# Kernel tuning notes

Hardware: AMD Instinct MI355X
Metric: run time of the kernel (lower is better)

## Reference

```python
import jax, jax.numpy as jnp
import numpy as np

EPS = 1e-5

def _ln(x, g, b):
    m = x.mean(-1, keepdims=True)
    v = jnp.var(x, axis=-1, keepdims=True)
    return (x - m) * jax.lax.rsqrt(v + EPS) * g + b

def _conv(x, w, b, stride=1, pad=1):
    y = jax.lax.conv_general_dilated(x, w, (stride, stride), [(pad, pad), (pad, pad)],
                                     dimension_numbers=('NCHW', 'OIHW', 'NCHW'))
    return y + b[None, :, None, None]

def _bn(x, g, b, m, v):
    # inference-mode BatchNorm2d
    inv = jax.lax.rsqrt(v + EPS)
    return (x - m[None, :, None, None]) * (g * inv)[None, :, None, None] + b[None, :, None, None]

def _sru_dir(u0, u1, u2, res, vf, vr, bf, br, reverse):
    # elementwise gated recurrence (SRU v2, identity activation, no dropout)
    def step(c, inp):
        a0, a1, a2, rx = inp
        f = jax.nn.sigmoid(a1 + vf * c + bf)
        c2 = f * c + (1.0 - f) * a0
        r = jax.nn.sigmoid(a2 + vr * c2 + br)
        return c2, r * c2 + (1.0 - r) * rx
    c0 = jnp.zeros_like(u0[0])
    _, hs = jax.lax.scan(step, c0, (u0, u1, u2, res), reverse=reverse)
    return hs

def _sru_layer(x, g, b, wp, w, vc, bias, k, h):
    # x: [L,B,n_in]; layer_norm on input, factored weight (projection), bidirectional
    xn = _ln(x, g, b)
    L, B, _ = xn.shape
    U = (xn @ wp) @ w                      # [L,B,2*k*h]
    U = U.reshape(L, B, 2, k, h)
    outs = []
    for d, rev in ((0, False), (1, True)):
        u = U[:, :, d]
        res = u[..., 3, :] if k == 4 else xn[..., d * h:(d + 1) * h]
        outs.append(_sru_dir(u[..., 0, :], u[..., 1, :], u[..., 2, :], res,
                             vc[d, 0], vc[d, 1], bias[d, 0], bias[d, 1], rev))
    return jnp.concatenate(outs, axis=-1)

def _forward(x, conv0_w, conv0_b, rconv1_w, rconv1_b, rbn1_g, rbn1_b, rbn1_m, rbn1_v,
             rconv2_w, rconv2_b, rbn2_g, rbn2_b, rbn2_m, rbn2_v,
             ln0_g, ln0_b, wproj0, w0, vc0, bias0, ln_g, ln_b, wproj, w, vc, bias,
             cln_g, cln_b, cls_w):
    H = 512
    h = _conv(x, conv0_w, conv0_b, stride=2)           # [B,32,F/2,T/2]
    for i in range(3):                                  # 3 residual blocks
        r = h
        h1 = jax.nn.relu(_bn(_conv(h, rconv1_w[i], rconv1_b[i]), rbn1_g[i], rbn1_b[i], rbn1_m[i], rbn1_v[i]))
        h2 = _bn(_conv(h1, rconv2_w[i], rconv2_b[i]), rbn2_g[i], rbn2_b[i], rbn2_m[i], rbn2_v[i])
        h = jax.nn.relu(h2 + r)
    Bb, C, Fr, Tt = h.shape
    s = h.reshape(Bb, C * Fr, Tt).transpose(2, 0, 1)   # [T,B,2048]
    s = _sru_layer(s, ln0_g, ln0_b, wproj0, w0, vc0, bias0, 4, H)  # layer 0: n_in != n_out -> k=4
    for i in range(3):                                  # layers 1..3: n_in == n_out -> k=3
        s = _sru_layer(s, ln_g[i], ln_b[i], wproj[i], w[i], vc[i], bias[i], 3, H)
    s = s.transpose(1, 0, 2)                            # [B,T,1024]
    s = _ln(s, cln_g, cln_b)
    return s @ cls_w                                    # [B,T,30]

def setup_inputs():
    key = jax.random.key(0)
    ks = iter(jax.random.split(key, 32))
    def nrm(shape, scale=1.0):
        return jax.random.normal(next(ks), shape, jnp.float32) * scale
    H, P, F2, D, hb = 512, 256, 2048, 1024, -2.0
    d = {}
    d['x'] = nrm((16, 1, 128, 2048))
    d['conv0_w'] = nrm((32, 1, 3, 3), (2.0 / 9) ** 0.5)
    d['conv0_b'] = jnp.zeros((32,))
    d['rconv1_w'] = nrm((3, 32, 32, 3, 3), (2.0 / (32 * 9)) ** 0.5)
    d['rconv1_b'] = jnp.zeros((3, 32))
    d['rbn1_g'] = jnp.ones((3, 32)); d['rbn1_b'] = jnp.zeros((3, 32))
    d['rbn1_m'] = nrm((3, 32), 0.1); d['rbn1_v'] = jnp.ones((3, 32))
    d['rconv2_w'] = nrm((3, 32, 32, 3, 3), (2.0 / (32 * 9)) ** 0.5)
    d['rconv2_b'] = jnp.zeros((3, 32))
    d['rbn2_g'] = 0.1 * jnp.ones((3, 32)); d['rbn2_b'] = jnp.zeros((3, 32))
    d['rbn2_m'] = nrm((3, 32), 0.1); d['rbn2_v'] = jnp.ones((3, 32))
    d['ln0_g'] = jnp.ones((F2,)); d['ln0_b'] = jnp.zeros((F2,))
    d['wproj0'] = nrm((F2, P), F2 ** -0.5)
    d['w0'] = nrm((P, 2 * 4 * H), P ** -0.5)
    d['vc0'] = nrm((2, 2, H), 0.1)
    d['bias0'] = jnp.zeros((2, 2, H)).at[:, 0].set(hb)
    d['ln_g'] = jnp.ones((3, D)); d['ln_b'] = jnp.zeros((3, D))
    d['wproj'] = nrm((3, D, P), D ** -0.5)
    d['w'] = nrm((3, P, 2 * 3 * H), P ** -0.5)
    d['vc'] = nrm((3, 2, 2, H), 0.1)
    d['bias'] = jnp.zeros((3, 2, 2, H)).at[:, :, 0].set(hb)
    d['cln_g'] = jnp.ones((D,)); d['cln_b'] = jnp.zeros((D,))
    d['cls_w'] = nrm((D, 30), D ** -0.5)
    return d

def reference(x, conv0_w, conv0_b, rconv1_w, rconv1_b, rbn1_g, rbn1_b, rbn1_m, rbn1_v,
              rconv2_w, rconv2_b, rbn2_g, rbn2_b, rbn2_m, rbn2_v,
              ln0_g, ln0_b, wproj0, w0, vc0, bias0, ln_g, ln_b, wproj, w, vc, bias,
              cln_g, cln_b, cls_w):
    return _forward(x, conv0_w, conv0_b, rconv1_w, rconv1_b, rbn1_g, rbn1_b, rbn1_m, rbn1_v,
                    rconv2_w, rconv2_b, rbn2_g, rbn2_b, rbn2_m, rbn2_v,
                    ln0_g, ln0_b, wproj0, w0, vc0, bias0, ln_g, ln_b, wproj, w, vc, bias,
                    cln_g, cln_b, cls_w)
```

## Files before the change

kernel.cpp:

```cpp
#include <hip/hip_runtime.h>
#include <hip/hip_bf16.h>
#include <math.h>

#define DEV __device__ __forceinline__

typedef __attribute__((ext_vector_type(8))) short short8;
typedef __attribute__((ext_vector_type(4))) float floatx4;

DEV float b2f_lo(unsigned u) { return __uint_as_float(u << 16); }
DEV float b2f_hi(unsigned u) { return __uint_as_float(u & 0xffff0000u); }

#if __has_builtin(__builtin_amdgcn_exp2f)
DEV float fexp2_(float x) { return __builtin_amdgcn_exp2f(x); }
#else
DEV float fexp2_(float x) { return exp2f(x); }
#endif
#if __has_builtin(__builtin_amdgcn_rcpf)
DEV float frcp_(float x) { return __builtin_amdgcn_rcpf(x); }
#else
DEV float frcp_(float x) { return 1.f / x; }
#endif

DEV void gl2lds16(const void* g, void* l) {
  __builtin_amdgcn_global_load_lds(
      (const __attribute__((address_space(1))) unsigned int*)g,
      (__attribute__((address_space(3))) unsigned int*)l, 16, 0, 0);
}

union U8 { uint4 u; __hip_bfloat16 h[8]; };

__global__ __launch_bounds__(256) void conv_stem_nhwc(const float* __restrict__ x,
    const float* __restrict__ w, const float* __restrict__ bias,
    __hip_bfloat16* __restrict__ out) {
  __shared__ float sX[3][2052];
  __shared__ float sW[288];
  __shared__ float sB[32];
  const int tid = threadIdx.x;
  const int f = blockIdx.x, n = blockIdx.y;
  const float* xb = x + (size_t)n * 262144;

  for (int i = tid; i < 1536; i += 256) {
    int r = i >> 9, c4 = i & 511;
    int fi = 2 * f - 1 + r;
    float4 v = {0.f, 0.f, 0.f, 0.f};
    if (fi >= 0 && fi < 128) v = *(const float4*)&xb[fi * 2048 + c4 * 4];
    sX[r][1 + c4 * 4 + 0] = v.x;
    sX[r][1 + c4 * 4 + 1] = v.y;
    sX[r][1 + c4 * 4 + 2] = v.z;
    sX[r][1 + c4 * 4 + 3] = v.w;
  }
  if (tid < 3) { sX[tid][0] = 0.f; sX[tid][2049] = 0.f; }
  for (int i = tid; i < 288; i += 256) sW[i] = w[i];
  if (tid < 32) sB[tid] = bias[tid];
  __syncthreads();

  float xv[4][9];
#pragma unroll
  for (int q = 0; q < 4; ++q) {
    int t = tid + q * 256;
#pragma unroll
    for (int r = 0; r < 3; ++r)
#pragma unroll
      for (int dc = 0; dc < 3; ++dc)
        xv[q][r * 3 + dc] = sX[r][2 * t + dc];
  }
#pragma unroll
  for (int ocq = 0; ocq < 4; ++ocq) {
    float wr[8][9];
#pragma unroll
    for (int oo = 0; oo < 8; ++oo)
#pragma unroll
      for (int qq = 0; qq < 9; ++qq)
        wr[oo][qq] = sW[(ocq * 8 + oo) * 9 + qq];
#pragma unroll
    for (int q = 0; q < 4; ++q) {
      U8 o;
#pragma unroll
      for (int oo = 0; oo < 8; ++oo) {
        float acc = sB[ocq * 8 + oo];
#pragma unroll
        for (int qq = 0; qq < 9; ++qq) acc = fmaf(wr[oo][qq], xv[q][qq], acc);
        o.h[oo] = __float2bfloat16(acc);
      }
      int t = tid + q * 256;
      *(uint4*)&out[(((size_t)n * 64 + f) * 1024 + t) * 32 + ocq * 8] = o.u;
    }
  }
}

__global__ __launch_bounds__(256) void wtap_conv6(const float* __restrict__ w1,
    const float* __restrict__ w2, __hip_bfloat16* __restrict__ out) {
  int i = blockIdx.x * 256 + threadIdx.x;
  if (i < 55296) {
    int b = i / 9216, r = i - b * 9216;
    int layer = b >> 1, which = b & 1;
    const float* src = (which ? w2 : w1) + layer * 9216;
    int tap = r >> 10, oc = (r >> 5) & 31, ic = r & 31;
    out[b * 9216 + r] = __float2bfloat16(src[(oc * 32 + ic) * 9 + tap]);
  }
}

template <int ADD>
__global__ __launch_bounds__(256) void conv_mfma(const __hip_bfloat16* __restrict__ Hin,
    const __hip_bfloat16* __restrict__ wt,
    const float* __restrict__ cb, const float* __restrict__ bg,
    const float* __restrict__ bb, const float* __restrict__ bm,
    const float* __restrict__ bv, __hip_bfloat16* Hres) {
  __shared__ __hip_bfloat16 sIn[6 * 66 * 40];
  __hip_bfloat16* sOut = sIn;
  const int tid = threadIdx.x;
  const int tb = blockIdx.x, fb = blockIdx.y, n = blockIdx.z;
  const int t0 = tb * 64, f0 = fb * 4;
  const __hip_bfloat16* Hb = Hin + (size_t)n * 2097152;

  for (int c = tid; c < 1584; c += 256) {
    int rr = c / 264;
    int r2 = c - rr * 264;
    int p = r2 >> 2, icq = r2 & 3;
    int fi = f0 - 1 + rr;
    int tg = t0 + p - 1;
    uint4 v = {0, 0, 0, 0};
    if (fi >= 0 && fi < 64 && tg >= 0 && tg < 1024)
      v = *(const uint4*)&Hb[((size_t)fi * 1024 + tg) * 32 + icq * 8];
    *(uint4*)&sIn[(rr * 66 + p) * 40 + icq * 8] = v;
  }

  const int lane = tid & 63, wave = tid >> 6;
  const int fr = lane & 15, fq = lane >> 4;
  short8 bfrag[9][2];
#pragma unroll
  for (int tap = 0; tap < 9; ++tap)
#pragma unroll
    for (int j = 0; j < 2; ++j)
      bfrag[tap][j] = *(const short8*)&wt[(tap * 32 + j * 16 + fr) * 32 + fq * 8];

  __syncthreads();

  const int tw = wave * 16;
  floatx4 acc[4][2];
#pragma unroll
  for (int fp = 0; fp < 4; ++fp)
#pragma unroll
    for (int j = 0; j < 2; ++j) acc[fp][j] = (floatx4){0.f, 0.f, 0.f, 0.f};

#pragma unroll
  for (int fp = 0; fp < 4; ++fp) {
    int pbase = tw + fr;
#pragma unroll
    for (int df = 0; df < 3; ++df)
#pragma unroll
      for (int dc = 0; dc < 3; ++dc) {
        short8 af =
            *(const short8*)&sIn[((fp + df) * 66 + pbase + dc) * 40 + fq * 8];
        acc[fp][0] = __builtin_amdgcn_mfma_f32_16x16x32_bf16(
            af, bfrag[df * 3 + dc][0], acc[fp][0], 0, 0, 0);
        acc[fp][1] = __builtin_amdgcn_mfma_f32_16x16x32_bf16(
            af, bfrag[df * 3 + dc][1], acc[fp][1], 0, 0, 0);
      }
  }

  float sc0 = bg[fr] * rsqrtf(bv[fr] + 1e-5f);
  float sh0 = (cb[fr] - bm[fr]) * sc0 + bb[fr];
  float sc1 = bg[fr + 16] * rsqrtf(bv[fr + 16] + 1e-5f);
  float sh1 = (cb[fr + 16] - bm[fr + 16]) * sc1 + bb[fr + 16];

  __syncthreads();
#pragma unroll
  for (int fp = 0; fp < 4; ++fp)
#pragma unroll
    for (int j = 0; j < 2; ++j) {
      float sc = j ? sc1 : sc0, sh = j ? sh1 : sh0;
#pragma unroll
      for (int reg = 0; reg < 4; ++reg) {
        int t_l = tw + fq * 4 + reg;
        sOut[(fp * 64 + t_l) * 40 + j * 16 + fr] =
            __float2bfloat16(acc[fp][j][reg] * sc + sh);
      }
    }
  __syncthreads();

  for (int c = tid; c < 1024; c += 256) {
    int fp = c >> 8, rem = c & 255;
    int t_l = rem >> 2, icq = rem & 3;
    U8 y;
    y.u = *(uint4*)&sOut[(fp * 64 + t_l) * 40 + icq * 8];
    size_t addr = (((size_t)n * 64 + f0 + fp) * 1024 + t0 + t_l) * 32 + icq * 8;
    U8 o;
    if (ADD) {
      U8 r;
      r.u = *(const uint4*)&Hres[addr];
#pragma unroll
      for (int i = 0; i < 8; ++i)
        o.h[i] = __float2bfloat16(
            fmaxf(__bfloat162float(y.h[i]) + __bfloat162float(r.h[i]), 0.f));
    } else {
#pragma unroll
      for (int i = 0; i < 8; ++i)
        o.h[i] = __float2bfloat16(fmaxf(__bfloat162float(y.h[i]), 0.f));
    }
    *(uint4*)&Hres[addr] = o.u;
  }
}

__global__ __launch_bounds__(256) void ln_nhwc(const __hip_bfloat16* __restrict__ H,
    const float* __restrict__ g, const float* __restrict__ b,
    __hip_bfloat16* __restrict__ xn) {
  int r = blockIdx.x;
  int t = r >> 4, n = r & 15;
  int tid = threadIdx.x;
  int f = tid >> 2, icq = tid & 3;
  U8 v;
  v.u = *(const uint4*)&H[(((size_t)n * 64 + f) * 1024 + t) * 32 + icq * 8];
  float xv[8];
  float sum = 0.f, ss = 0.f;
#pragma unroll
  for (int i = 0; i < 8; ++i) {
    xv[i] = __bfloat162float(v.h[i]);
    sum += xv[i];
    ss += xv[i] * xv[i];
  }
#pragma unroll
  for (int off = 32; off > 0; off >>= 1) {
    sum += __shfl_down(sum, off);
    ss  += __shfl_down(ss, off);
  }
  __shared__ float red[8];
  int lane = tid & 63, wave = tid >> 6;
  if (lane == 0) { red[wave] = sum; red[4 + wave] = ss; }
  __syncthreads();
  sum = red[0] + red[1] + red[2] + red[3];
  ss  = red[4] + red[5] + red[6] + red[7];
  float mean = sum * (1.f / 2048.f);
  float var = ss * (1.f / 2048.f) - mean * mean;
  float inv = rsqrtf(var + 1e-5f);
  U8 o;
#pragma unroll
  for (int i = 0; i < 8; ++i) {
    int cf = (icq * 8 + i) * 64 + f;
    o.h[i] = __float2bfloat16((xv[i] - mean) * inv * g[cf] + b[cf]);
  }
  *(uint4*)&xn[(size_t)r * 2048 + tid * 8] = o.u;
}

__global__ __launch_bounds__(256) void wt_perm0(const float* __restrict__ in,
    __hip_bfloat16* __restrict__ out) {
  int i = blockIdx.x * 256 + threadIdx.x;
  int p = i >> 11, kp = i & 2047;
  int ic = kp & 31, f = kp >> 5;
  out[i] = __float2bfloat16(in[(ic * 64 + f) * 256 + p]);
}

__global__ __launch_bounds__(256) void ln_rows_h(const __hip_bfloat16* __restrict__ in,
    const float* __restrict__ g, const float* __restrict__ b,
    __hip_bfloat16* __restrict__ out) {
  int r = blockIdx.x;
  int tid = threadIdx.x;
  union { ushort4 u; __hip_bfloat16 h[4]; } iv;
  iv.u = *(const ushort4*)&in[(size_t)r * 1024 + tid * 4];
  float x0 = __bfloat162float(iv.h[0]);
  float x1 = __bfloat162float(iv.h[1]);
  float x2 = __bfloat162float(iv.h[2]);
  float x3 = __bfloat162float(iv.h[3]);
  float sum = x0 + x1 + x2 + x3;
  float ss = x0 * x0 + x1 * x1 + x2 * x2 + x3 * x3;
#pragma unroll
  for (int off = 32; off > 0; off >>= 1) {
    sum += __shfl_down(sum, off);
    ss  += __shfl_down(ss, off);
  }
  __shared__ float red[8];
  int lane = tid & 63, wave = tid >> 6;
  if (lane == 0) { red[wave] = sum; red[4 + wave] = ss; }
  __syncthreads();
  sum = red[0] + red[1] + red[2] + red[3];
  ss  = red[4] + red[5] + red[6] + red[7];
  float mean = sum * (1.f / 1024.f);
  float var = ss * (1.f / 1024.f) - mean * mean;
  float inv = rsqrtf(var + 1e-5f);
  float4 gv = *(const float4*)&g[tid * 4];
  float4 bv = *(const float4*)&b[tid * 4];
  union { ushort4 u; __hip_bfloat16 h[4]; } o;
  o.h[0] = __float2bfloat16((x0 - mean) * inv * gv.x + bv.x);
  o.h[1] = __float2bfloat16((x1 - mean) * inv * gv.y + bv.y);
  o.h[2] = __float2bfloat16((x2 - mean) * inv * gv.z + bv.z);
  o.h[3] = __float2bfloat16((x3 - mean) * inv * gv.w + bv.w);
  *(ushort4*)&out[(size_t)r * 1024 + tid * 4] = o.u;
}

__global__ __launch_bounds__(256) void wt_bf16(const float* __restrict__ in,
    __hip_bfloat16* __restrict__ out, int K, int N, int inStride, int outStride) {
  __shared__ float tile[32][33];
  int x = threadIdx.x, y0 = threadIdx.y;
  int bn = blockIdx.x * 32;
  int bk = blockIdx.y * 32;
  const float* src = in + (size_t)blockIdx.z * inStride;
  __hip_bfloat16* dst = out + (size_t)blockIdx.z * outStride;
#pragma unroll
  for (int i = 0; i < 4; ++i) {
    int yy = y0 + i * 8;
    tile[yy][x] = src[(size_t)(bk + yy) * N + bn + x];
  }
  __syncthreads();
#pragma unroll
  for (int i = 0; i < 4; ++i) {
    int yy = y0 + i * 8;
    dst[(size_t)(bn + yy) * K + bk + x] = __float2bfloat16(tile[x][yy]);
  }
}

__global__ void wexp_prep(const float* __restrict__ in,
    __hip_bfloat16* __restrict__ out, int korig, int inStride, int outStride) {
  __shared__ float tile[32][33];
  int jt = blockIdx.x;
  int ckt = blockIdx.y;
  int z = blockIdx.z;
  int layer = z >> 3, dk = z & 7;
  int d = dk >> 2, k = dk & 3;
  if (k >= korig) return;
  const float* src = in + (size_t)layer * inStride;
  __hip_bfloat16* dst = out + (size_t)layer * outStride;
  int x = threadIdx.x, y0 = threadIdx.y;
#pragma unroll
  for (int i = 0; i < 4; ++i) {
    int yy = y0 + i * 8;
    tile[yy][x] = src[(size_t)(ckt * 32 + yy) * (korig * 1024) +
                      (d * korig + k) * 512 + jt * 32 + x];
  }
  __syncthreads();
#pragma unroll
  for (int i = 0; i < 4; ++i) {
    int yy = y0 + i * 8;
    int j = jt * 32 + yy;
    int rIdx;
    if (korig == 4)
      rIdx = (d * 512 + j) * 4 + k;
    else
      rIdx = (k < 2) ? ((d * 512 + j) * 2 + k) : (2048 + d * 512 + j);
    dst[(size_t)rIdx * 256 + ckt * 32 + x] = __float2bfloat16(tile[x][yy]);
  }
}

__global__ __launch_bounds__(256) void wct_prep(const float* __restrict__ in,
    __hip_bfloat16* __restrict__ out) {
  int i = blockIdx.x * 256 + threadIdx.x;
  int nn = i >> 10, kk = i & 1023;
  out[i] = __float2bfloat16(nn < 30 ? in[kk * 30 + nn] : 0.f);
}

__global__ __launch_bounds__(256) void gemm_bf16(const __hip_bfloat16* __restrict__ A,
    const __hip_bfloat16* __restrict__ Bt, __hip_bfloat16* __restrict__ C,
    int M, int N, int K) {
  __shared__ __hip_bfloat16 As[128 * 32];
  __shared__ __hip_bfloat16 Bs[128 * 32];
  const int tid = threadIdx.x;
  const int m0 = blockIdx.y * 128, n0 = blockIdx.x * 128;
  const int lane = tid & 63, wave = tid >> 6;
  const int wm = wave & 1, wn = wave >> 1;
  const int fr = lane & 15, fq = lane >> 4;
  const int srow = lane >> 2, sch = lane & 3;

  const __hip_bfloat16* ga0 = &A[(size_t)(m0 + wave * 32 + srow) * K + sch * 8];
  const __hip_bfloat16* ga1 = ga0 + (size_t)16 * K;
  const __hip_bfloat16* gb0 = &Bt[(size_t)(n0 + wave * 32 + srow) * K + sch * 8];
  const __hip_bfloat16* gb1 = gb0 + (size_t)16 * K;
  __hip_bfloat16* la0 = &As[(wave * 32) * 32];
  __hip_bfloat16* la1 = &As[(wave * 32 + 16) * 32];
  __hip_bfloat16* lb0 = &Bs[(wave * 32) * 32];
  __hip_bfloat16* lb1 = &Bs[(wave * 32 + 16) * 32];

  floatx4 acc[4][4];
#pragma unroll
  for (int i = 0; i < 4; ++i)
#pragma unroll
    for (int j = 0; j < 4; ++j)
      acc[i][j] = (floatx4){0.f, 0.f, 0.f, 0.f};

  for (int k0 = 0; k0 < K; k0 += 32) {
    __syncthreads();
    gl2lds16(ga0 + k0, la0);
    gl2lds16(ga1 + k0, la1);
    gl2lds16(gb0 + k0, lb0);
    gl2lds16(gb1 + k0, lb1);
    __syncthreads();

    short8 af[4], bf_[4];
#pragma unroll
    for (int i = 0; i < 4; ++i) {
      af[i]  = *(const short8*)&As[(wm * 64 + i * 16 + fr) * 32 + fq * 8];
      bf_[i] = *(const short8*)&Bs[(wn * 64 + i * 16 + fr) * 32 + fq * 8];
    }
#pragma unroll
    for (int i = 0; i < 4; ++i)
#pragma unroll
      for (int j = 0; j < 4; ++j)
        acc[i][j] = __builtin_amdgcn_mfma_f32_16x16x32_bf16(af[i], bf_[j],
                                                            acc[i][j], 0, 0, 0);
  }

#pragma unroll
  for (int i = 0; i < 4; ++i)
#pragma unroll
    for (int j = 0; j < 4; ++j)
#pragma unroll
      for (int reg = 0; reg < 4; ++reg) {
        int row = m0 + wm * 64 + i * 16 + fq * 4 + reg;
        int col = n0 + wn * 64 + j * 16 + fr;
        C[(size_t)row * N + col] = __float2bfloat16(acc[i][j][reg]);
      }
}

__global__ __launch_bounds__(256) void cls_gemm(const __hip_bfloat16* __restrict__ A,
    const __hip_bfloat16* __restrict__ Wct, float* __restrict__ out) {
  const int tid = threadIdx.x;
  const int lane = tid & 63, wave = tid >> 6;
  const int fr = lane & 15, fq = lane >> 4;
  const int m0 = (blockIdx.x * 4 + wave) * 16;
  floatx4 acc[2];
  acc[0] = (floatx4){0.f, 0.f, 0.f, 0.f};
  acc[1] = (floatx4){0.f, 0.f, 0.f, 0.f};
#pragma unroll 4
  for (int k0 = 0; k0 < 1024; k0 += 32) {
    short8 af = *(const short8*)&A[(size_t)(m0 + fr) * 1024 + k0 + fq * 8];
    short8 b0 = *(const short8*)&Wct[(size_t)fr * 1024 + k0 + fq * 8];
    short8 b1 = *(const short8*)&Wct[(size_t)(16 + fr) * 1024 + k0 + fq * 8];
    acc[0] = __builtin_amdgcn_mfma_f32_16x16x32_bf16(af, b0, acc[0], 0, 0, 0);
    acc[1] = __builtin_amdgcn_mfma_f32_16x16x32_bf16(af, b1, acc[1], 0, 0, 0);
  }
#pragma unroll
  for (int j = 0; j < 2; ++j) {
    int col = j * 16 + fr;
    if (col < 30) {
#pragma unroll
      for (int reg = 0; reg < 4; ++reg) {
        int row = m0 + fq * 4 + reg;
        int t = row >> 4, n = row & 15;
        out[(size_t)n * 30720 + t * 30 + col] = acc[j][reg];
      }
    }
  }
}

__global__ __launch_bounds__(64) void sru_scan4(const __hip_bfloat16* __restrict__ U,
    const float* __restrict__ vc, const float* __restrict__ bias,
    __hip_bfloat16* __restrict__ out) {
  int gid = blockIdx.x * 64 + threadIdx.x;
  int j = gid & 511;
  int n = (gid >> 9) & 15;
  int d = gid >> 13;
  const float NL2E = -1.44269504f;
  float vf2 = NL2E * vc[(d * 2 + 0) * 512 + j];
  float vr2 = NL2E * vc[(d * 2 + 1) * 512 + j];
  float bf2 = NL2E * bias[(d * 2 + 0) * 512 + j];
  float br2 = NL2E * bias[(d * 2 + 1) * 512 + j];

  const char* Ub = (const char*)(U + (size_t)n * 4096 + d * 2048) + (size_t)j * 8;
  char* Ob = (char*)(out + (size_t)n * 1024 + d * 512) + (size_t)j * 2;
  const int US = d ? -131072 : 131072;
  const int OS = d ? -32768 : 32768;
  int uoff = d ? 1023 * 131072 : 0;
  int ooff = d ? 1023 * 32768 : 0;

  uint2 B0[16], B1[16], B2[16], B3[16];
  float c = 0.f;

#define LOADC(UB)                                                         \
  {                                                                       \
    _Pragma("unroll") for (int ss = 0; ss < 16; ++ss) {                   \
      UB[ss] = *(const uint2*)(Ub + uoff);                                \
      uoff += US;                                                         \
    }                                                                     \
  }

#define COMPC(UB)                                                         \
  {                                                                       \
    _Pragma("unroll") for (int ss = 0; ss < 16; ++ss) {                   \
      uint2 uv = UB[ss];                                                  \
      float a0 = b2f_lo(uv.x), a1 = b2f_hi(uv.x), a2 = b2f_lo(uv.y);      \
      float rx = b2f_hi(uv.y);                                            \
      float A1 = fmaf(a1, NL2E, bf2);                                     \
      float f = frcp_(1.f + fexp2_(fmaf(vf2, c, A1)));                    \
      float c2 = fmaf(f, c - a0, a0);                                     \
      float A2 = fmaf(a2, NL2E, br2);                                     \
      float r = frcp_(1.f + fexp2_(fmaf(vr2, c2, A2)));                   \
      float y = fmaf(r, c2 - rx, rx);                                     \
      *(__hip_bfloat16*)(Ob + ooff) = __float2bfloat16(y);                \
      ooff += OS;                                                         \
      c = c2;                                                             \
    }                                                                     \
  }

  LOADC(B0);
  LOADC(B1);
  LOADC(B2);
  for (int cb = 0; cb < 64; cb += 4) {
    LOADC(B3);
    COMPC(B0);
    if (cb + 4 < 64) LOADC(B0);
    COMPC(B1);
    if (cb + 5 < 64) LOADC(B1);
    COMPC(B2);
    if (cb + 6 < 64) LOADC(B2);
    COMPC(B3);
  }
#undef LOADC
#undef COMPC
}

__global__ __launch_bounds__(64) void sru_scan3(const __hip_bfloat16* __restrict__ U,
    const __hip_bfloat16* __restrict__ xn,
    const float* __restrict__ vc, const float* __restrict__ bias,
    __hip_bfloat16* __restrict__ out) {
  int gid = blockIdx.x * 64 + threadIdx.x;
  int j = gid & 511;
  int n = (gid >> 9) & 15;
  int d = gid >> 13;
  const float NL2E = -1.44269504f;
  float vf2 = NL2E * vc[(d * 2 + 0) * 512 + j];
  float vr2 = NL2E * vc[(d * 2 + 1) * 512 + j];
  float bf2 = NL2E * bias[(d * 2 + 0) * 512 + j];
  float br2 = NL2E * bias[(d * 2 + 1) * 512 + j];

  const char* Ub01 = (const char*)U + (size_t)n * 6144 + (size_t)(d * 512 + j) * 4;
  const char* Ub2  = (const char*)U + (size_t)n * 6144 +
                     (size_t)(2048 + d * 512 + j) * 2;
  const char* Xb = (const char*)xn + (size_t)n * 2048 + (size_t)(d * 512 + j) * 2;
  char* Ob = (char*)(out + (size_t)n * 1024 + d * 512) + (size_t)j * 2;
  const int US = d ? -98304 : 98304;
  const int XS = d ? -32768 : 32768;
  const int OS = d ? -32768 : 32768;
  int uoff = d ? 1023 * 98304 : 0;
  int u2off = uoff;
  int xoff = d ? 1023 * 32768 : 0;
  int ooff = xoff;

  uint B0u[16], B1u[16], B2u[16], B3u[16];
  ushort B0a[16], B1a[16], B2a[16], B3a[16];
  ushort B0x[16], B1x[16], B2x[16], B3x[16];
  float c = 0.f;

#define LOADC(Bu, Ba, Bx)                                                 \
  {                                                                       \
    _Pragma("unroll") for (int ss = 0; ss < 16; ++ss) {                   \
      Bu[ss] = *(const uint*)(Ub01 + uoff);                               \
      Ba[ss] = *(const ushort*)(Ub2 + u2off);                             \
      Bx[ss] = *(const ushort*)(Xb + xoff);                               \
      uoff += US;                                                         \
      u2off += US;                                                        \
      xoff += XS;                                                         \
    }                                                                     \
  }

#define COMPC(Bu, Ba, Bx)                                                 \
  {                                                                       \
    _Pragma("unroll") for (int ss = 0; ss < 16; ++ss) {                   \
      float a0 = b2f_lo(Bu[ss]), a1 = b2f_hi(Bu[ss]);                     \
      float a2 = __uint_as_float((uint)Ba[ss] << 16);                     \
      float rx = __uint_as_float((uint)Bx[ss] << 16);                     \
      float A1 = fmaf(a1, NL2E, bf2);                                     \
      float f = frcp_(1.f + fexp2_(fmaf(vf2, c, A1)));                    \
      float c2 = fmaf(f, c - a0, a0);                                     \
      float A2 = fmaf(a2, NL2E, br2);                                     \
      float r = frcp_(1.f + fexp2_(fmaf(vr2, c2, A2)));                   \
      float y = fmaf(r, c2 - rx, rx);                                     \
      *(__hip_bfloat16*)(Ob + ooff) = __float2bfloat16(y);                \
      ooff += OS;                                                         \
      c = c2;                                                             \
    }                                                                     \
  }

  LOADC(B0u, B0a, B0x);
  LOADC(B1u, B1a, B1x);
  LOADC(B2u, B2a, B2x);
  for (int cb = 0; cb < 64; cb += 4) {
    LOADC(B3u, B3a, B3x);
    COMPC(B0u, B0a, B0x);
    if (cb + 4 < 64) LOADC(B0u, B0a, B0x);
    COMPC(B1u, B1a, B1x);
    if (cb + 5 < 64) LOADC(B1u, B1a, B1x);
    COMPC(B2u, B2a, B2x);
    if (cb + 6 < 64) LOADC(B2u, B2a, B2x);
    COMPC(B3u, B3a, B3x);
  }
#undef LOADC
#undef COMPC
}

extern "C" void kernel_launch(void* const* d_in, const int* in_sizes, int n_in,
                              void* d_out, int out_size, void* d_ws, size_t ws_size,
                              hipStream_t stream) {
  const float* x        = (const float*)d_in[0];
  const float* conv0_w  = (const float*)d_in[1];
  const float* conv0_b  = (const float*)d_in[2];
  const float* rconv1_w = (const float*)d_in[3];
  const float* rconv1_b = (const float*)d_in[4];
  const float* rbn1_g   = (const float*)d_in[5];
  const float* rbn1_b   = (const float*)d_in[6];
  const float* rbn1_m   = (const float*)d_in[7];
  const float* rbn1_v   = (const float*)d_in[8];
  const float* rconv2_w = (const float*)d_in[9];
  const float* rconv2_b = (const float*)d_in[10];
  const float* rbn2_g   = (const float*)d_in[11];
  const float* rbn2_b   = (const float*)d_in[12];
  const float* rbn2_m   = (const float*)d_in[13];
  const float* rbn2_v   = (const float*)d_in[14];
  const float* ln0_g    = (const float*)d_in[15];
  const float* ln0_b    = (const float*)d_in[16];
  const float* wproj0   = (const float*)d_in[17];
  const float* w0       = (const float*)d_in[18];
  const float* vc0      = (const float*)d_in[19];
  const float* bias0    = (const float*)d_in[20];
  const float* ln_g     = (const float*)d_in[21];
  const float* ln_b     = (const float*)d_in[22];
  const float* wproj    = (const float*)d_in[23];
  const float* w        = (const float*)d_in[24];
  const float* vc       = (const float*)d_in[25];
  const float* bias     = (const float*)d_in[26];
  const float* cln_g    = (const float*)d_in[27];
  const float* cln_b    = (const float*)d_in[28];
  const float* cls_w    = (const float*)d_in[29];
  float* out = (float*)d_out;

  float* Af = (float*)d_ws;
  float* Bf = Af + 33554432;
  __hip_bfloat16* Ah = (__hip_bfloat16*)Af;
  __hip_bfloat16* Bh = (__hip_bfloat16*)Bf;

  __hip_bfloat16* hA     = Ah;
  __hip_bfloat16* hB     = Bh;
  __hip_bfloat16* wt_all = Ah + 62914560;
  __hip_bfloat16* Wp0t   = Ah + 52428800;

  __hip_bfloat16* s2h  = Bh;
  __hip_bfloat16* xnc  = Bh + 16777216;
  __hip_bfloat16* xn3  = Bh + 33554432;
  __hip_bfloat16* tmp  = Bh + 50331648;
  __hip_bfloat16* W3p  = Bh + 54525952;
  __hip_bfloat16* W0p  = Bh + 57671680;
  __hip_bfloat16* Wpt3 = Bh + 58720256;
  __hip_bfloat16* xn0  = Bh;
  __hip_bfloat16* U    = Ah;
  __hip_bfloat16* Wct  = Ah;

  wtap_conv6<<<216, 256, 0, stream>>>(rconv1_w, rconv2_w, wt_all);
  wt_perm0<<<2048, 256, 0, stream>>>(wproj0, Wp0t);
  wexp_prep<<<dim3(16, 8, 8), dim3(32, 8), 0, stream>>>(w0, W0p, 4, 0, 0);
  wexp_prep<<<dim3(16, 8, 24), dim3(32, 8), 0, stream>>>(w, W3p, 3,
                                                         786432, 786432);
  wt_bf16<<<dim3(8, 32, 3), dim3(32, 8), 0, stream>>>(wproj, Wpt3, 1024, 256,
                                                      262144, 262144);

  conv_stem_nhwc<<<dim3(64, 16), 256, 0, stream>>>(x, conv0_w, conv0_b, hA);
  for (int i = 0; i < 3; ++i) {
    conv_mfma<0><<<dim3(16, 16, 16), 256, 0, stream>>>(hA, wt_all + (i * 2) * 9216,
        rconv1_b + i * 32, rbn1_g + i * 32, rbn1_b + i * 32,
        rbn1_m + i * 32, rbn1_v + i * 32, hB);
    conv_mfma<1><<<dim3(16, 16, 16), 256, 0, stream>>>(hB, wt_all + (i * 2 + 1) * 9216,
        rconv2_b + i * 32, rbn2_g + i * 32, rbn2_b + i * 32,
        rbn2_m + i * 32, rbn2_v + i * 32, hA);
  }

  ln_nhwc<<<16384, 256, 0, stream>>>(hA, ln0_g, ln0_b, xn0);
  gemm_bf16<<<dim3(2, 128), 256, 0, stream>>>(xn0, Wp0t, tmp, 16384, 256, 2048);
  gemm_bf16<<<dim3(32, 128), 256, 0, stream>>>(tmp, W0p, U, 16384, 4096, 256);
  sru_scan4<<<256, 64, 0, stream>>>(U, vc0, bias0, s2h);

  for (int i = 0; i < 3; ++i) {
    ln_rows_h<<<16384, 256, 0, stream>>>(s2h, ln_g + i * 1024, ln_b + i * 1024, xn3);
    gemm_bf16<<<dim3(2, 128), 256, 0, stream>>>(xn3, Wpt3 + i * 262144, tmp,
                                                16384, 256, 1024);
    gemm_bf16<<<dim3(24, 128), 256, 0, stream>>>(tmp, W3p + i * 786432, U,
                                                 16384, 3072, 256);
    sru_scan3<<<256, 64, 0, stream>>>(U, xn3, vc + i * 2048, bias + i * 2048, s2h);
  }

  ln_rows_h<<<16384, 256, 0, stream>>>(s2h, cln_g, cln_b, xnc);
  wct_prep<<<128, 256, 0, stream>>>(cls_w, Wct);
  cls_gemm<<<256, 256, 0, stream>>>(xnc, Wct, out);
}
```

Measured before the change: 1.166 ms.

## Split SRU scan into serial c-recurrence and fused parallel output+layernorm

The SRU recurrence kernel now computes only the serial cell state c, and reads just a0 and the pre-scaled forget gate input per step. The reset gate, highway output and the next layer's layernorm move into a fully parallel per-row kernel. Gate bias and the -log2e scaling are folded into the GEMM epilogue through a per-column scale/bias table, and the weight layout is permuted so the scan reads 4 bytes per step instead of 8. This shortens the latency-bound serial scan and removes the separate layernorm pass, at the cost of an extra c2 buffer write and read.

```diff
diff --git a/kernel.cpp b/kernel.cpp
--- a/kernel.cpp
+++ b/kernel.cpp
@@ -250,43 +250,6 @@
   out[i] = __float2bfloat16(in[(ic * 64 + f) * 256 + p]);
 }
 
-__global__ __launch_bounds__(256) void ln_rows_h(const __hip_bfloat16* __restrict__ in,
-    const float* __restrict__ g, const float* __restrict__ b,
-    __hip_bfloat16* __restrict__ out) {
-  int r = blockIdx.x;
-  int tid = threadIdx.x;
-  union { ushort4 u; __hip_bfloat16 h[4]; } iv;
-  iv.u = *(const ushort4*)&in[(size_t)r * 1024 + tid * 4];
-  float x0 = __bfloat162float(iv.h[0]);
-  float x1 = __bfloat162float(iv.h[1]);
-  float x2 = __bfloat162float(iv.h[2]);
-  float x3 = __bfloat162float(iv.h[3]);
-  float sum = x0 + x1 + x2 + x3;
-  float ss = x0 * x0 + x1 * x1 + x2 * x2 + x3 * x3;
-#pragma unroll
-  for (int off = 32; off > 0; off >>= 1) {
-    sum += __shfl_down(sum, off);
-    ss  += __shfl_down(ss, off);
-  }
-  __shared__ float red[8];
-  int lane = tid & 63, wave = tid >> 6;
-  if (lane == 0) { red[wave] = sum; red[4 + wave] = ss; }
-  __syncthreads();
-  sum = red[0] + red[1] + red[2] + red[3];
-  ss  = red[4] + red[5] + red[6] + red[7];
-  float mean = sum * (1.f / 1024.f);
-  float var = ss * (1.f / 1024.f) - mean * mean;
-  float inv = rsqrtf(var + 1e-5f);
-  float4 gv = *(const float4*)&g[tid * 4];
-  float4 bv = *(const float4*)&b[tid * 4];
-  union { ushort4 u; __hip_bfloat16 h[4]; } o;
-  o.h[0] = __float2bfloat16((x0 - mean) * inv * gv.x + bv.x);
-  o.h[1] = __float2bfloat16((x1 - mean) * inv * gv.y + bv.y);
-  o.h[2] = __float2bfloat16((x2 - mean) * inv * gv.z + bv.z);
-  o.h[3] = __float2bfloat16((x3 - mean) * inv * gv.w + bv.w);
-  *(ushort4*)&out[(size_t)r * 1024 + tid * 4] = o.u;
-}
-
 __global__ __launch_bounds__(256) void wt_bf16(const float* __restrict__ in,
     __hip_bfloat16* __restrict__ out, int K, int N, int inStride, int outStride) {
   __shared__ float tile[32][33];
@@ -330,14 +293,48 @@
 #pragma unroll
   for (int i = 0; i < 4; ++i) {
     int yy = y0 + i * 8;
-    int j = jt * 32 + yy;
+    int ch = d * 512 + jt * 32 + yy;
     int rIdx;
     if (korig == 4)
-      rIdx = (d * 512 + j) * 4 + k;
+      rIdx = (k < 2) ? (ch * 2 + k) : (2048 + ch * 2 + (k - 2));
     else
-      rIdx = (k < 2) ? ((d * 512 + j) * 2 + k) : (2048 + d * 512 + j);
+      rIdx = (k < 2) ? (ch * 2 + k) : (2048 + ch);
     dst[(size_t)rIdx * 256 + ckt * 32 + x] = __float2bfloat16(tile[x][yy]);
   }
+}
+
+__global__ __launch_bounds__(256) void colsb_prep(const float* __restrict__ bias0,
+    const float* __restrict__ bias3, float2* __restrict__ out) {
+  int i = blockIdx.x * 256 + threadIdx.x;
+  if (i >= 13312) return;
+  const float NL2E = -1.44269504f;
+  float s = 1.f, bb = 0.f;
+  if (i < 4096) {
+    int col = i;
+    if (col < 2048) {
+      int ch = col >> 1, e = col & 1;
+      int d = ch >> 9, jj = ch & 511;
+      if (e) { s = NL2E; bb = NL2E * bias0[d * 1024 + jj]; }
+    } else {
+      int cc = col - 2048, ch = cc >> 1, e = cc & 1;
+      int d = ch >> 9, jj = ch & 511;
+      if (!e) { s = NL2E; bb = NL2E * bias0[d * 1024 + 512 + jj]; }
+    }
+  } else {
+    int rem = i - 4096;
+    int layer = rem / 3072, col = rem - layer * 3072;
+    const float* bsrc = bias3 + layer * 2048;
+    if (col < 2048) {
+      int ch = col >> 1, e = col & 1;
+      int d = ch >> 9, jj = ch & 511;
+      if (e) { s = NL2E; bb = NL2E * bsrc[d * 1024 + jj]; }
+    } else {
+      int ch = col - 2048;
+      int d = ch >> 9, jj = ch & 511;
+      s = NL2E; bb = NL2E * bsrc[d * 1024 + 512 + jj];
+    }
+  }
+  out[i] = make_float2(s, bb);
 }
 
 __global__ __launch_bounds__(256) void wct_prep(const float* __restrict__ in,
@@ -349,7 +346,7 @@
 
 __global__ __launch_bounds__(256) void gemm_bf16(const __hip_bfloat16* __restrict__ A,
     const __hip_bfloat16* __restrict__ Bt, __hip_bfloat16* __restrict__ C,
-    int M, int N, int K) {
+    const float2* __restrict__ csb, int M, int N, int K) {
   __shared__ __hip_bfloat16 As[128 * 32];
   __shared__ __hip_bfloat16 Bs[128 * 32];
   const int tid = threadIdx.x;
@@ -400,13 +397,16 @@
 #pragma unroll
   for (int i = 0; i < 4; ++i)
 #pragma unroll
-    for (int j = 0; j < 4; ++j)
+    for (int j = 0; j < 4; ++j) {
+      int col = n0 + wn * 64 + j * 16 + fr;
+      float s = 1.f, sb = 0.f;
+      if (csb) { float2 t = csb[col]; s = t.x; sb = t.y; }
 #pragma unroll
       for (int reg = 0; reg < 4; ++reg) {
         int row = m0 + wm * 64 + i * 16 + fq * 4 + reg;
-        int col = n0 + wn * 64 + j * 16 + fr;
-        C[(size_t)row * N + col] = __float2bfloat16(acc[i][j][reg]);
+        C[(size_t)row * N + col] = __float2bfloat16(fmaf(acc[i][j][reg], s, sb));
       }
+    }
 }
 
 __global__ __launch_bounds__(256) void cls_gemm(const __hip_bfloat16* __restrict__ A,
@@ -440,33 +440,30 @@
   }
 }
 
-__global__ __launch_bounds__(64) void sru_scan4(const __hip_bfloat16* __restrict__ U,
-    const float* __restrict__ vc, const float* __restrict__ bias,
-    __hip_bfloat16* __restrict__ out) {
+template <int ROWB>
+__global__ __launch_bounds__(64) void scan_c(const __hip_bfloat16* __restrict__ U,
+    const float* __restrict__ vc, __hip_bfloat16* __restrict__ c2out) {
   int gid = blockIdx.x * 64 + threadIdx.x;
   int j = gid & 511;
   int n = (gid >> 9) & 15;
   int d = gid >> 13;
   const float NL2E = -1.44269504f;
-  float vf2 = NL2E * vc[(d * 2 + 0) * 512 + j];
-  float vr2 = NL2E * vc[(d * 2 + 1) * 512 + j];
-  float bf2 = NL2E * bias[(d * 2 + 0) * 512 + j];
-  float br2 = NL2E * bias[(d * 2 + 1) * 512 + j];
-
-  const char* Ub = (const char*)(U + (size_t)n * 4096 + d * 2048) + (size_t)j * 8;
-  char* Ob = (char*)(out + (size_t)n * 1024 + d * 512) + (size_t)j * 2;
-  const int US = d ? -131072 : 131072;
+  float vf2 = NL2E * vc[d * 1024 + j];
+
+  const char* Ub = (const char*)U + (size_t)n * ROWB + (size_t)(d * 512 + j) * 4;
+  char* Ob = (char*)c2out + (size_t)n * 2048 + (size_t)(d * 512 + j) * 2;
+  const int US = d ? -(16 * ROWB) : (16 * ROWB);
   const int OS = d ? -32768 : 32768;
-  int uoff = d ? 1023 * 131072 : 0;
+  int uoff = d ? 1023 * 16 * ROWB : 0;
   int ooff = d ? 1023 * 32768 : 0;
 
-  uint2 B0[16], B1[16], B2[16], B3[16];
+  uint B0[16], B1[16], B2[16], B3[16];
   float c = 0.f;
 
 #define LOADC(UB)                                                         \
   {                                                                       \
     _Pragma("unroll") for (int ss = 0; ss < 16; ++ss) {                   \
-      UB[ss] = *(const uint2*)(Ub + uoff);                                \
+      UB[ss] = *(const uint*)(Ub + uoff);                                 \
       uoff += US;                                                         \
     }                                                                     \
   }
@@ -474,18 +471,12 @@
 #define COMPC(UB)                                                         \
   {                                                                       \
     _Pragma("unroll") for (int ss = 0; ss < 16; ++ss) {                   \
-      uint2 uv = UB[ss];                                                  \
-      float a0 = b2f_lo(uv.x), a1 = b2f_hi(uv.x), a2 = b2f_lo(uv.y);      \
-      float rx = b2f_hi(uv.y);                                            \
-      float A1 = fmaf(a1, NL2E, bf2);                                     \
-      float f = frcp_(1.f + fexp2_(fmaf(vf2, c, A1)));                    \
-      float c2 = fmaf(f, c - a0, a0);                                     \
-      float A2 = fmaf(a2, NL2E, br2);                                     \
-      float r = frcp_(1.f + fexp2_(fmaf(vr2, c2, A2)));                   \
-      float y = fmaf(r, c2 - rx, rx);                                     \
-      *(__hip_bfloat16*)(Ob + ooff) = __float2bfloat16(y);                \
+      uint u = UB[ss];                                                    \
+      float a0 = b2f_lo(u), a1p = b2f_hi(u);                              \
+      float f = frcp_(1.f + fexp2_(fmaf(vf2, c, a1p)));                   \
+      c = fmaf(f, c - a0, a0);                                            \
+      *(__hip_bfloat16*)(Ob + ooff) = __float2bfloat16(c);                \
       ooff += OS;                                                         \
-      c = c2;                                                             \
     }                                                                     \
   }
 
@@ -506,83 +497,69 @@
 #undef COMPC
 }
 
-__global__ __launch_bounds__(64) void sru_scan3(const __hip_bfloat16* __restrict__ U,
-    const __hip_bfloat16* __restrict__ xn,
-    const float* __restrict__ vc, const float* __restrict__ bias,
-    __hip_bfloat16* __restrict__ out) {
-  int gid = blockIdx.x * 64 + threadIdx.x;
-  int j = gid & 511;
-  int n = (gid >> 9) & 15;
-  int d = gid >> 13;
+template <int K4>
+__global__ __launch_bounds__(256) void yln(const __hip_bfloat16* __restrict__ c2buf,
+    const __hip_bfloat16* __restrict__ U, const __hip_bfloat16* __restrict__ xn,
+    const float* __restrict__ vc, const float* __restrict__ g,
+    const float* __restrict__ b, __hip_bfloat16* __restrict__ outx) {
+  int r = blockIdx.x;
+  int tid = threadIdx.x;
+  int ch0 = tid * 4;
   const float NL2E = -1.44269504f;
-  float vf2 = NL2E * vc[(d * 2 + 0) * 512 + j];
-  float vr2 = NL2E * vc[(d * 2 + 1) * 512 + j];
-  float bf2 = NL2E * bias[(d * 2 + 0) * 512 + j];
-  float br2 = NL2E * bias[(d * 2 + 1) * 512 + j];
-
-  const char* Ub01 = (const char*)U + (size_t)n * 6144 + (size_t)(d * 512 + j) * 4;
-  const char* Ub2  = (const char*)U + (size_t)n * 6144 +
-                     (size_t)(2048 + d * 512 + j) * 2;
-  const char* Xb = (const char*)xn + (size_t)n * 2048 + (size_t)(d * 512 + j) * 2;
-  char* Ob = (char*)(out + (size_t)n * 1024 + d * 512) + (size_t)j * 2;
-  const int US = d ? -98304 : 98304;
-  const int XS = d ? -32768 : 32768;
-  const int OS = d ? -32768 : 32768;
-  int uoff = d ? 1023 * 98304 : 0;
-  int u2off = uoff;
-  int xoff = d ? 1023 * 32768 : 0;
-  int ooff = xoff;
-
-  uint B0u[16], B1u[16], B2u[16], B3u[16];
-  ushort B0a[16], B1a[16], B2a[16], B3a[16];
-  ushort B0x[16], B1x[16], B2x[16], B3x[16];
-  float c = 0.f;
-
-#define LOADC(Bu, Ba, Bx)                                                 \
-  {                                                                       \
-    _Pragma("unroll") for (int ss = 0; ss < 16; ++ss) {                   \
-      Bu[ss] = *(const uint*)(Ub01 + uoff);                               \
-      Ba[ss] = *(const ushort*)(Ub2 + u2off);                             \
-      Bx[ss] = *(const ushort*)(Xb + xoff);                               \
-      uoff += US;                                                         \
-      u2off += US;                                                        \
-      xoff += XS;                                                         \
-    }                                                                     \
-  }
-
-#define COMPC(Bu, Ba, Bx)                                                 \
-  {                                                                       \
-    _Pragma("unroll") for (int ss = 0; ss < 16; ++ss) {                   \
-      float a0 = b2f_lo(Bu[ss]), a1 = b2f_hi(Bu[ss]);                     \
-      float a2 = __uint_as_float((uint)Ba[ss] << 16);                     \
-      float rx = __uint_as_float((uint)Bx[ss] << 16);                     \
-      float A1 = fmaf(a1, NL2E, bf2);                                     \
-      float f = frcp_(1.f + fexp2_(fmaf(vf2, c, A1)));                    \
-      float c2 = fmaf(f, c - a0, a0);                                     \
-      float A2 = fmaf(a2, NL2E, br2);                                     \
-      float r = frcp_(1.f + fexp2_(fmaf(vr2, c2, A2)));                   \
-      float y = fmaf(r, c2 - rx, rx);                                     \
-      *(__hip_bfloat16*)(Ob + ooff) = __float2bfloat16(y);                \
-      ooff += OS;                                                         \
-      c = c2;                                                             \
-    }                                                                     \
-  }
-
-  LOADC(B0u, B0a, B0x);
-  LOADC(B1u, B1a, B1x);
-  LOADC(B2u, B2a, B2x);
-  for (int cb = 0; cb < 64; cb += 4) {
-    LOADC(B3u, B3a, B3x);
-    COMPC(B0u, B0a, B0x);
-    if (cb + 4 < 64) LOADC(B0u, B0a, B0x);
-    COMPC(B1u, B1a, B1x);
-    if (cb + 5 < 64) LOADC(B1u, B1a, B1x);
-    COMPC(B2u, B2a, B2x);
-    if (cb + 6 < 64) LOADC(B2u, B2a, B2x);
-    COMPC(B3u, B3a, B3x);
-  }
-#undef LOADC
-#undef COMPC
+
+  union { ushort4 u; __hip_bfloat16 h[4]; } cv;
+  cv.u = *(const ushort4*)&c2buf[(size_t)r * 1024 + ch0];
+  float a2p[4], rx[4];
+  if (K4) {
+    uint4 pr = *(const uint4*)((const char*)U + (size_t)r * 8192 + 4096 + tid * 16);
+    uint pp[4] = {pr.x, pr.y, pr.z, pr.w};
+#pragma unroll
+    for (int i = 0; i < 4; ++i) { a2p[i] = b2f_lo(pp[i]); rx[i] = b2f_hi(pp[i]); }
+  } else {
+    union { ushort4 u; __hip_bfloat16 h[4]; } av, xv;
+    av.u = *(const ushort4*)((const char*)U + (size_t)r * 6144 + 4096 + tid * 8);
+    xv.u = *(const ushort4*)&xn[(size_t)r * 1024 + ch0];
+#pragma unroll
+    for (int i = 0; i < 4; ++i) {
+      a2p[i] = __bfloat162float(av.h[i]);
+      rx[i]  = __bfloat162float(xv.h[i]);
+    }
+  }
+
+  int d = ch0 >> 9, j0 = ch0 & 511;
+  float y[4], sum = 0.f, ss = 0.f;
+#pragma unroll
+  for (int i = 0; i < 4; ++i) {
+    float vr2 = NL2E * vc[d * 1024 + 512 + j0 + i];
+    float cc = __bfloat162float(cv.h[i]);
+    float rr = frcp_(1.f + fexp2_(fmaf(vr2, cc, a2p[i])));
+    y[i] = fmaf(rr, cc - rx[i], rx[i]);
+    sum += y[i];
+    ss += y[i] * y[i];
+  }
+#pragma unroll
+  for (int off = 32; off > 0; off >>= 1) {
+    sum += __shfl_down(sum, off);
+    ss  += __shfl_down(ss, off);
+  }
+  __shared__ float red[8];
+  int lane = tid & 63, wave = tid >> 6;
+  if (lane == 0) { red[wave] = sum; red[4 + wave] = ss; }
+  __syncthreads();
+  sum = red[0] + red[1] + red[2] + red[3];
+  ss  = red[4] + red[5] + red[6] + red[7];
+  float mean = sum * (1.f / 1024.f);
+  float var = ss * (1.f / 1024.f) - mean * mean;
+  float inv = rsqrtf(var + 1e-5f);
+  float4 gv = *(const float4*)&g[ch0];
+  float4 bv = *(const float4*)&b[ch0];
+  float gg[4] = {gv.x, gv.y, gv.z, gv.w};
+  float bb[4] = {bv.x, bv.y, bv.z, bv.w};
+  union { ushort4 u; __hip_bfloat16 h[4]; } o;
+#pragma unroll
+  for (int i = 0; i < 4; ++i)
+    o.h[i] = __float2bfloat16((y[i] - mean) * inv * gg[i] + bb[i]);
+  *(ushort4*)&outx[(size_t)r * 1024 + ch0] = o.u;
 }
 
 extern "C" void kernel_launch(void* const* d_in, const int* in_sizes, int n_in,
@@ -630,16 +607,20 @@
   __hip_bfloat16* wt_all = Ah + 62914560;
   __hip_bfloat16* Wp0t   = Ah + 52428800;
 
-  __hip_bfloat16* s2h  = Bh;
+  __hip_bfloat16* c2   = Bh;
   __hip_bfloat16* xnc  = Bh + 16777216;
   __hip_bfloat16* xn3  = Bh + 33554432;
   __hip_bfloat16* tmp  = Bh + 50331648;
   __hip_bfloat16* W3p  = Bh + 54525952;
   __hip_bfloat16* W0p  = Bh + 57671680;
   __hip_bfloat16* Wpt3 = Bh + 58720256;
+  float2* csb          = (float2*)(Bh + 59506688);
   __hip_bfloat16* xn0  = Bh;
   __hip_bfloat16* U    = Ah;
   __hip_bfloat16* Wct  = Ah;
+
+  const float2* csb4 = csb;
+  const float2* csb3 = csb + 4096;
 
   wtap_conv6<<<216, 256, 0, stream>>>(rconv1_w, rconv2_w, wt_all);
   wt_perm0<<<2048, 256, 0, stream>>>(wproj0, Wp0t);
@@ -648,6 +629,7 @@
                                                          786432, 786432);
   wt_bf16<<<dim3(8, 32, 3), dim3(32, 8), 0, stream>>>(wproj, Wpt3, 1024, 256,
                                                       262144, 262144);
+  colsb_prep<<<52, 256, 0, stream>>>(bias0, bias, csb);
 
   conv_stem_nhwc<<<dim3(64, 16), 256, 0, stream>>>(x, conv0_w, conv0_b, hA);
   for (int i = 0; i < 3; ++i) {
@@ -660,20 +642,27 @@
   }
 
   ln_nhwc<<<16384, 256, 0, stream>>>(hA, ln0_g, ln0_b, xn0);
-  gemm_bf16<<<dim3(2, 128), 256, 0, stream>>>(xn0, Wp0t, tmp, 16384, 256, 2048);
-  gemm_bf16<<<dim3(32, 128), 256, 0, stream>>>(tmp, W0p, U, 16384, 4096, 256);
-  sru_scan4<<<256, 64, 0, stream>>>(U, vc0, bias0, s2h);
+  gemm_bf16<<<dim3(2, 128), 256, 0, stream>>>(xn0, Wp0t, tmp, nullptr,
+                                              16384, 256, 2048);
+  gemm_bf16<<<dim3(32, 128), 256, 0, stream>>>(tmp, W0p, U, csb4,
+                                               16384, 4096, 256);
+  scan_c<8192><<<256, 64, 0, stream>>>(U, vc0, c2);
+  __hip_bfloat16* xnA = xn3;
+  __hip_bfloat16* xnB = xnc;
+  yln<1><<<16384, 256, 0, stream>>>(c2, U, nullptr, vc0, ln_g, ln_b, xnA);
 
   for (int i = 0; i < 3; ++i) {
-    ln_rows_h<<<16384, 256, 0, stream>>>(s2h, ln_g + i * 1024, ln_b + i * 1024, xn3);
-    gemm_bf16<<<dim3(2, 128), 256, 0, stream>>>(xn3, Wpt3 + i * 262144, tmp,
-                                                16384, 256, 1024);
+    gemm_bf16<<<dim3(2, 128), 256, 0, stream>>>(xnA, Wpt3 + i * 262144, tmp,
+                                                nullptr, 16384, 256, 1024);
     gemm_bf16<<<dim3(24, 128), 256, 0, stream>>>(tmp, W3p + i * 786432, U,
-                                                 16384, 3072, 256);
-    sru_scan3<<<256, 64, 0, stream>>>(U, xn3, vc + i * 2048, bias + i * 2048, s2h);
-  }
-
-  ln_rows_h<<<16384, 256, 0, stream>>>(s2h, cln_g, cln_b, xnc);
+                                                 csb3 + i * 3072, 16384, 3072, 256);
+    scan_c<6144><<<256, 64, 0, stream>>>(U, vc + i * 2048, c2);
+    const float* gg = (i < 2) ? (ln_g + (i + 1) * 1024) : cln_g;
+    const float* bb = (i < 2) ? (ln_b + (i + 1) * 1024) : cln_b;
+    yln<0><<<16384, 256, 0, stream>>>(c2, U, xnA, vc + i * 2048, gg, bb, xnB);
+    __hip_bfloat16* sw = xnA; xnA = xnB; xnB = sw;
+  }
+
   wct_prep<<<128, 256, 0, stream>>>(cls_w, Wct);
-  cls_gemm<<<256, 256, 0, stream>>>(xnc, Wct, out);
-}
+  cls_gemm<<<256, 256, 0, stream>>>(xnA, Wct, out);
+}
```

New measurement: 1.106 ms. -5.1%, faster.
